# Performance work log

Hardware: AMD Instinct MI355X
Metric: run time of the kernel (lower is better)

The kernel has to match this reference:

```python
import jax, jax.numpy as jnp
import numpy as np

N, E, F_IN, D, H = 20000, 640000, 128, 16, 8  # nodes, edges, in_features, out_features, n_heads


def _linear_params(k, fan_in, fan_out):
    W = jax.random.normal(k, (fan_in, fan_out), jnp.float32) / np.sqrt(fan_in)
    b = jnp.zeros((fan_out,), jnp.float32)
    return W, b


def setup_inputs() -> dict:
    key = jax.random.key(0)
    ks = jax.random.split(key, 8)
    x = jax.random.normal(ks[0], (N, F_IN), jnp.float32)
    edge_index = jax.random.randint(ks[1], (2, E), 0, N, dtype=jnp.int64)
    Wq, bq = _linear_params(ks[2], F_IN, D * H)
    Wk, bk = _linear_params(ks[3], F_IN, D * H)
    Wv, bv = _linear_params(ks[4], F_IN, D * H)
    Wpsi, bpsi = _linear_params(ks[5], D, D)
    Wo, bo = _linear_params(ks[6], D * H * 2, F_IN)
    gamma = jnp.ones((F_IN,), jnp.float32)
    beta = jnp.zeros((F_IN,), jnp.float32)
    return {"x": x, "edge_index": edge_index, "Wq": Wq, "bq": bq, "Wk": Wk, "bk": bk,
            "Wv": Wv, "bv": bv, "Wpsi": Wpsi, "bpsi": bpsi, "Wo": Wo, "bo": bo,
            "gamma": gamma, "beta": beta}


def _segment_softmax(logits, seg, num_segments):
    # numerically-stable softmax of edge logits grouped by destination node (row)
    m = jax.ops.segment_max(logits, seg, num_segments=num_segments)  # [N,H]
    m = jnp.where(jnp.isfinite(m), m, 0.0)
    e = jnp.exp(logits - m[seg])  # [E,H]
    s = jax.ops.segment_sum(e, seg, num_segments=num_segments)  # [N,H]
    return e / (s[seg] + 1e-16)


def reference(x, edge_index, Wq, bq, Wk, bk, Wv, bv, Wpsi, bpsi, Wo, bo, gamma, beta):
    q = (x @ Wq + bq).reshape(N, H, D)
    k = (x @ Wk + bk).reshape(N, H, D)
    v = (x @ Wv + bv).reshape(N, H, D)
    row, col = edge_index[0], edge_index[1]

    logits = jnp.einsum('ehd,ehd->eh', q[row], k[col]) / np.sqrt(D)  # [E,H]
    alpha = _segment_softmax(logits, row, N)  # [E,H]

    v_j = v[col]  # [E,H,D]
    h_lp = jax.ops.segment_sum((alpha[..., None] * v_j).reshape(E, H * D), row, num_segments=N)
    v_bp = jnp.tanh(v_j @ Wpsi + bpsi)  # per-head linear on last dim, [E,H,D]
    h_bp = jax.ops.segment_sum((alpha[..., None] * v_bp).reshape(E, H * D), row, num_segments=N)

    h_out = jnp.concatenate([h_lp, h_bp], axis=1) @ Wo + bo  # [N,F_IN]
    y = x + jax.nn.relu(h_out)
    mu = jnp.mean(y, axis=-1, keepdims=True)
    var = jnp.mean(jnp.square(y - mu), axis=-1, keepdims=True)
    return (y - mu) * jax.lax.rsqrt(var + 1e-5) * gamma + beta
```

## Files before the change

kernel.cpp:

```cpp
#include <hip/hip_runtime.h>
#include <hip/hip_bf16.h>
#include <math.h>

#define NN 20000
#define EE 640000

typedef __attribute__((ext_vector_type(8))) short short8;
typedef __attribute__((ext_vector_type(4))) float f32x4;
typedef __hip_bfloat16 bf16;
typedef __hip_bfloat162 bf162;

__device__ inline ushort f2bf(float f) {
  bf16 h = __float2bfloat16(f);
  return *(ushort*)&h;
}
__device__ inline float2 ldbf2(const ushort* p) {
  return __bfloat1622float2(*(const bf162*)p);
}

__global__ __launch_bounds__(256) void qkv_mfma(
    const float* __restrict__ x,
    const float* __restrict__ Wq, const float* __restrict__ bq,
    const float* __restrict__ Wk, const float* __restrict__ bk,
    const float* __restrict__ Wv, const float* __restrict__ bv,
    float* __restrict__ qbuf, ushort* __restrict__ kvb) {
  __shared__ ushort As[128 * 136];
  __shared__ ushort Bts[128 * 136];
  int t = threadIdx.x;
  int n0 = blockIdx.x * 128;
  int mat = blockIdx.y;
  const float* W    = mat == 0 ? Wq : (mat == 1 ? Wk : Wv);
  const float* bias = mat == 0 ? bq : (mat == 1 ? bk : bv);

  {
    int r = t >> 1, half = (t & 1) * 64;
    int n = n0 + r;
    ushort* dst = &As[r * 136 + half];
    if (n < NN) {
      const float* src = x + (size_t)n * 128 + half;
#pragma unroll
      for (int j = 0; j < 8; ++j) {
        float4 f0 = *(const float4*)(src + 8 * j);
        float4 f1 = *(const float4*)(src + 8 * j + 4);
        ushort tmp[8] = {f2bf(f0.x), f2bf(f0.y), f2bf(f0.z), f2bf(f0.w),
                         f2bf(f1.x), f2bf(f1.y), f2bf(f1.z), f2bf(f1.w)};
        *(uint4*)(dst + 8 * j) = *(uint4*)tmp;
      }
    } else {
#pragma unroll
      for (int j = 0; j < 8; ++j) *(uint4*)(dst + 8 * j) = make_uint4(0, 0, 0, 0);
    }
  }
  {
    int k = t >> 1, nh = (t & 1) * 64;
    const float* src = W + (size_t)k * 128 + nh;
#pragma unroll
    for (int i = 0; i < 16; ++i) {
      float4 f = *(const float4*)(src + 4 * i);
      Bts[(nh + 4 * i + 0) * 136 + k] = f2bf(f.x);
      Bts[(nh + 4 * i + 1) * 136 + k] = f2bf(f.y);
      Bts[(nh + 4 * i + 2) * 136 + k] = f2bf(f.z);
      Bts[(nh + 4 * i + 3) * 136 + k] = f2bf(f.w);
    }
  }
  __syncthreads();

  int w = t >> 6, lane = t & 63;
  int m = lane & 15, q = lane >> 4;
  int r0 = w * 32;
  f32x4 acc0[8], acc1[8];
#pragma unroll
  for (int c = 0; c < 8; ++c) {
    acc0[c] = (f32x4){0.f, 0.f, 0.f, 0.f};
    acc1[c] = (f32x4){0.f, 0.f, 0.f, 0.f};
  }
#pragma unroll
  for (int kb = 0; kb < 4; ++kb) {
    int kof = kb * 32 + 8 * q;
    short8 a0 = *(const short8*)&As[(r0 + m) * 136 + kof];
    short8 a1 = *(const short8*)&As[(r0 + 16 + m) * 136 + kof];
#pragma unroll
    for (int c = 0; c < 8; ++c) {
      short8 b = *(const short8*)&Bts[(c * 16 + m) * 136 + kof];
      acc0[c] = __builtin_amdgcn_mfma_f32_16x16x32_bf16(a0, b, acc0[c], 0, 0, 0);
      acc1[c] = __builtin_amdgcn_mfma_f32_16x16x32_bf16(a1, b, acc1[c], 0, 0, 0);
    }
  }
  int koff = (mat == 2) ? 128 : 0;
#pragma unroll
  for (int c = 0; c < 8; ++c) {
    int col = c * 16 + m;
    float bb = bias[col];
#pragma unroll
    for (int reg = 0; reg < 4; ++reg) {
      int row0 = n0 + r0 + 4 * q + reg;
      int row1 = row0 + 16;
      float v0 = acc0[c][reg] + bb;
      float v1 = acc1[c][reg] + bb;
      if (mat == 0) {
        if (row0 < NN) qbuf[(size_t)row0 * 128 + col] = v0;
        if (row1 < NN) qbuf[(size_t)row1 * 128 + col] = v1;
      } else {
        if (row0 < NN) kvb[(size_t)row0 * 384 + koff + col] = f2bf(v0);
        if (row1 < NN) kvb[(size_t)row1 * 384 + koff + col] = f2bf(v1);
      }
    }
  }
}

__global__ __launch_bounds__(256) void vb_kernel(
    ushort* __restrict__ kvb,
    const float* __restrict__ Wpsi, const float* __restrict__ bpsi) {
  __shared__ float Ws[256];
  __shared__ float bs[16];
  int t = threadIdx.x;
  Ws[t] = Wpsi[t];
  if (t < 16) bs[t] = bpsi[t];
  __syncthreads();
  int idx = blockIdx.x * 256 + t;
  int n = idx >> 3, h = idx & 7;
  ushort* base = kvb + (size_t)n * 384;
  const ushort* vp = base + 128 + h * 16;
  float v[16];
#pragma unroll
  for (int j = 0; j < 8; ++j) {
    float2 f = ldbf2(vp + 2 * j);
    v[2 * j] = f.x; v[2 * j + 1] = f.y;
  }
  float o[16];
#pragma unroll
  for (int d = 0; d < 16; ++d) o[d] = bs[d];
#pragma unroll
  for (int dp = 0; dp < 16; ++dp) {
    float vv = v[dp];
#pragma unroll
    for (int d = 0; d < 16; ++d) o[d] = fmaf(vv, Ws[dp * 16 + d], o[d]);
  }
  ushort* dst = base + 256 + h * 16;
#pragma unroll
  for (int j = 0; j < 8; ++j) {
    uint u = (uint)f2bf(tanhf(o[2 * j])) | ((uint)f2bf(tanhf(o[2 * j + 1])) << 16);
    *(uint*)(dst + 2 * j) = u;
  }
}

__global__ __launch_bounds__(256) void scatter_pad(const int* __restrict__ ei,
                                                   int* __restrict__ cursor,
                                                   int* __restrict__ scol) {
  int e = blockIdx.x * 256 + threadIdx.x;
  if (e < EE) {
    int r = ei[e];
    int c = ei[EE + e];
    int pos = atomicAdd(&cursor[r], 1);
    if (pos < 128) scol[r * 128 + pos] = c;
  }
}

__global__ __launch_bounds__(256) void aggregate_kernel(
    const float* __restrict__ qbuf, const ushort* __restrict__ kvb,
    const int* __restrict__ cursor, const int* __restrict__ scol,
    float* __restrict__ hbuf) {
  int wid = threadIdx.x >> 6, lane = threadIdx.x & 63;
  int node = blockIdx.x * 4 + wid;
  int h = lane >> 3, dg = (lane & 7) * 2;
  int off = h * 16 + dg;
  const float SC = 0.25f * 1.44269504f;
  float2 q2 = *(const float2*)(qbuf + (size_t)node * 128 + off);
  q2.x *= SC; q2.y *= SC;
  int cnt = cursor[node];
  cnt = cnt > 128 ? 128 : cnt;
  int base = node * 128;
  float s = 0.f, aV0 = 0.f, aV1 = 0.f, aB0 = 0.f, aB1 = 0.f;

  auto proc = [&](int j) {
    const ushort* B = kvb + (size_t)j * 384 + off;
    float2 kk = ldbf2(B);
    float2 vv = ldbf2(B + 128);
    float2 tb = ldbf2(B + 256);
    float d = fmaf(q2.x, kk.x, q2.y * kk.y);
    d += __shfl_xor(d, 1);
    d += __shfl_xor(d, 2);
    d += __shfl_xor(d, 4);
    float wgt = exp2f(d);
    s += wgt;
    aV0 = fmaf(wgt, vv.x, aV0); aV1 = fmaf(wgt, vv.y, aV1);
    aB0 = fmaf(wgt, tb.x, aB0); aB1 = fmaf(wgt, tb.y, aB1);
  };
  int i = 0;
  for (; i + 4 <= cnt; i += 4) {
    int4 js = *(const int4*)&scol[base + i];
    proc(js.x); proc(js.y); proc(js.z); proc(js.w);
  }
  for (; i < cnt; ++i) proc(scol[base + i]);

  float inv = s > 0.f ? 1.f / s : 0.f;
  float* hp = hbuf + (size_t)node * 256 + off;
  *(float2*)(hp)       = make_float2(aV0 * inv, aV1 * inv);
  *(float2*)(hp + 128) = make_float2(aB0 * inv, aB1 * inv);
}

__global__ __launch_bounds__(256) void output_mfma(
    const float* __restrict__ hbuf, const float* __restrict__ x,
    const float* __restrict__ Wo, const float* __restrict__ bo,
    const float* __restrict__ gamma, const float* __restrict__ beta,
    float* __restrict__ out) {
  __shared__ ushort As[128 * 136];
  __shared__ ushort Bts[128 * 136];
  __shared__ float bos[128], gs[128], bts[128];
  int t = threadIdx.x;
  int n0 = blockIdx.x * 128;
  if (t < 128) { bos[t] = bo[t]; gs[t] = gamma[t]; bts[t] = beta[t]; }
  int w = t >> 6, lane = t & 63;
  int m = lane & 15, q = lane >> 4;
  int r0 = w * 32;
  f32x4 acc0[8], acc1[8];
#pragma unroll
  for (int c = 0; c < 8; ++c) {
    acc0[c] = (f32x4){0.f, 0.f, 0.f, 0.f};
    acc1[c] = (f32x4){0.f, 0.f, 0.f, 0.f};
  }
  for (int kc = 0; kc < 2; ++kc) {
    if (kc) __syncthreads();
    {
      int r = t >> 1, half = (t & 1) * 64;
      int n = n0 + r;
      ushort* dst = &As[r * 136 + half];
      if (n < NN) {
        const float* src = hbuf + (size_t)n * 256 + kc * 128 + half;
#pragma unroll
        for (int j = 0; j < 8; ++j) {
          float4 f0 = *(const float4*)(src + 8 * j);
          float4 f1 = *(const float4*)(src + 8 * j + 4);
          ushort tmp[8] = {f2bf(f0.x), f2bf(f0.y), f2bf(f0.z), f2bf(f0.w),
                           f2bf(f1.x), f2bf(f1.y), f2bf(f1.z), f2bf(f1.w)};
          *(uint4*)(dst + 8 * j) = *(uint4*)tmp;
        }
      } else {
#pragma unroll
        for (int j = 0; j < 8; ++j) *(uint4*)(dst + 8 * j) = make_uint4(0, 0, 0, 0);
      }
    }
    {
      int k = t >> 1, nh = (t & 1) * 64;
      const float* src = Wo + (size_t)(kc * 128 + k) * 128 + nh;
#pragma unroll
      for (int i = 0; i < 16; ++i) {
        float4 f = *(const float4*)(src + 4 * i);
        Bts[(nh + 4 * i + 0) * 136 + k] = f2bf(f.x);
        Bts[(nh + 4 * i + 1) * 136 + k] = f2bf(f.y);
        Bts[(nh + 4 * i + 2) * 136 + k] = f2bf(f.z);
        Bts[(nh + 4 * i + 3) * 136 + k] = f2bf(f.w);
      }
    }
    __syncthreads();
#pragma unroll
    for (int kb = 0; kb < 4; ++kb) {
      int kof = kb * 32 + 8 * q;
      short8 a0 = *(const short8*)&As[(r0 + m) * 136 + kof];
      short8 a1 = *(const short8*)&As[(r0 + 16 + m) * 136 + kof];
#pragma unroll
      for (int c = 0; c < 8; ++c) {
        short8 b = *(const short8*)&Bts[(c * 16 + m) * 136 + kof];
        acc0[c] = __builtin_amdgcn_mfma_f32_16x16x32_bf16(a0, b, acc0[c], 0, 0, 0);
        acc1[c] = __builtin_amdgcn_mfma_f32_16x16x32_bf16(a1, b, acc1[c], 0, 0, 0);
      }
    }
  }
#pragma unroll
  for (int half = 0; half < 2; ++half) {
#pragma unroll
    for (int reg = 0; reg < 4; ++reg) {
      int row = n0 + r0 + half * 16 + 4 * q + reg;
      bool valid = row < NN;
      float vals[8];
      float sum = 0.f;
#pragma unroll
      for (int c = 0; c < 8; ++c) {
        int col = c * 16 + m;
        float a = (half ? acc1[c][reg] : acc0[c][reg]) + bos[col];
        a = fmaxf(a, 0.f);
        float xv = valid ? x[(size_t)row * 128 + col] : 0.f;
        float v = a + xv;
        vals[c] = v;
        sum += v;
      }
      sum += __shfl_xor(sum, 1); sum += __shfl_xor(sum, 2);
      sum += __shfl_xor(sum, 4); sum += __shfl_xor(sum, 8);
      float mean = sum * (1.f / 128.f);
      float ssq = 0.f;
#pragma unroll
      for (int c = 0; c < 8; ++c) {
        float d = vals[c] - mean;
        ssq = fmaf(d, d, ssq);
      }
      ssq += __shfl_xor(ssq, 1); ssq += __shfl_xor(ssq, 2);
      ssq += __shfl_xor(ssq, 4); ssq += __shfl_xor(ssq, 8);
      float rstd = rsqrtf(ssq * (1.f / 128.f) + 1e-5f);
      if (valid) {
#pragma unroll
        for (int c = 0; c < 8; ++c) {
          int col = c * 16 + m;
          out[(size_t)row * 128 + col] = (vals[c] - mean) * rstd * gs[col] + bts[col];
        }
      }
    }
  }
}

extern "C" void kernel_launch(void* const* d_in, const int* in_sizes, int n_in,
                              void* d_out, int out_size, void* d_ws, size_t ws_size,
                              hipStream_t stream) {
  const float* x     = (const float*)d_in[0];
  const int*   ei    = (const int*)d_in[1];
  const float* Wq    = (const float*)d_in[2];
  const float* bq    = (const float*)d_in[3];
  const float* Wk    = (const float*)d_in[4];
  const float* bk    = (const float*)d_in[5];
  const float* Wv    = (const float*)d_in[6];
  const float* bv    = (const float*)d_in[7];
  const float* Wpsi  = (const float*)d_in[8];
  const float* bpsi  = (const float*)d_in[9];
  const float* Wo    = (const float*)d_in[10];
  const float* bo    = (const float*)d_in[11];
  const float* gamma = (const float*)d_in[12];
  const float* beta  = (const float*)d_in[13];
  float* out = (float*)d_out;

  char* ws = (char*)d_ws;
  float*  qbuf   = (float*) (ws);
  ushort* kvb    = (ushort*)(ws + 10240000);
  float*  hbuf   = (float*) (ws + 25600000);
  int*    cursor = (int*)   (ws + 46080000);
  int*    scol   = (int*)   (ws + 46160000);

  hipMemsetAsync(cursor, 0, 80000, stream);

  qkv_mfma<<<dim3(157, 3), 256, 0, stream>>>(x, Wq, bq, Wk, bk, Wv, bv, qbuf, kvb);
  vb_kernel<<<625, 256, 0, stream>>>(kvb, Wpsi, bpsi);
  scatter_pad<<<2500, 256, 0, stream>>>(ei, cursor, scol);
  aggregate_kernel<<<5000, 256, 0, stream>>>(qbuf, kvb, cursor, scol, hbuf);
  output_mfma<<<157, 256, 0, stream>>>(hbuf, x, Wo, bo, gamma, beta, out);
}
```

Baseline: 229.1 us.

## Pre-convert inputs to bf16, fold Wpsi into V GEMM, restructure aggregation

Adds a prep kernel that converts x and the weight matrices to bf16 in transposed layout once, so the MFMA kernels read fragments straight from global memory without LDS staging. The separate psi kernel is removed by precomputing Wv@Wpsi and a combined bias, which lets a fourth qkv GEMM slice produce tanh(v@Wpsi) directly. Aggregation now gives each lane group one edge with 16-wide vector loads, reduces across lanes with shuffles at the end, and writes h in bf16 to halve that traffic. The costs are an extra launch, an extra pass over x, rounding the folded weights to bf16, and direct global fragment loads in the GEMMs that may be less coalesced.

```diff
diff --git a/kernel.cpp b/kernel.cpp
--- a/kernel.cpp
+++ b/kernel.cpp
@@ -8,66 +8,127 @@
 typedef __attribute__((ext_vector_type(8))) short short8;
 typedef __attribute__((ext_vector_type(4))) float f32x4;
 typedef __hip_bfloat16 bf16;
-typedef __hip_bfloat162 bf162;
 
 __device__ inline ushort f2bf(float f) {
   bf16 h = __float2bfloat16(f);
   return *(ushort*)&h;
 }
-__device__ inline float2 ldbf2(const ushort* p) {
-  return __bfloat1622float2(*(const bf162*)p);
+__device__ inline float bflo(uint u) { return __uint_as_float(u << 16); }
+__device__ inline float bfhi(uint u) { return __uint_as_float(u & 0xFFFF0000u); }
+
+__global__ __launch_bounds__(256) void prep_kernel(
+    const float* __restrict__ x,
+    const float* __restrict__ Wq, const float* __restrict__ Wk,
+    const float* __restrict__ Wv, const float* __restrict__ Wo,
+    const float* __restrict__ Wpsi, const float* __restrict__ bpsi,
+    const float* __restrict__ bv,
+    ushort* __restrict__ xb, ushort* __restrict__ Wts ,
+    ushort* __restrict__ Wot, float* __restrict__ bvpsi) {
+  __shared__ float T[128][129];
+  __shared__ float WpsiS[256];
+  __shared__ float bpsiS[16];
+  int b = blockIdx.x, t = threadIdx.x;
+
+  if (b < 1250) {
+    int idx = b * 2048 + t * 8;
+    const float* src = x + idx;
+    float4 f0 = *(const float4*)(src);
+    float4 f1 = *(const float4*)(src + 4);
+    ushort tmp[8] = {f2bf(f0.x), f2bf(f0.y), f2bf(f0.z), f2bf(f0.w),
+                     f2bf(f1.x), f2bf(f1.y), f2bf(f1.z), f2bf(f1.w)};
+    *(uint4*)(xb + idx) = *(uint4*)tmp;
+    return;
+  }
+
+  if (b <= 1254) {
+    int which = b - 1250;
+    const float* W;
+    int k0 = 0;
+    if (which < 3) W = (which == 0) ? Wq : (which == 1 ? Wk : Wv);
+    else { W = Wo; k0 = (which - 3) * 128; }
+    {
+      int r = t >> 1, c0 = (t & 1) * 64;
+      const float* src = W + (size_t)(k0 + r) * 128 + c0;
+#pragma unroll
+      for (int j = 0; j < 16; ++j) {
+        float4 f = *(const float4*)(src + 4 * j);
+        T[r][c0 + 4 * j + 0] = f.x; T[r][c0 + 4 * j + 1] = f.y;
+        T[r][c0 + 4 * j + 2] = f.z; T[r][c0 + 4 * j + 3] = f.w;
+      }
+    }
+    __syncthreads();
+    int n = t >> 1, kh = (t & 1) * 64;
+    if (which < 3) {
+      ushort* dst = Wts + which * 16384 + n * 128 + kh;
+#pragma unroll
+      for (int j8 = 0; j8 < 8; ++j8) {
+        ushort buf[8];
+#pragma unroll
+        for (int j = 0; j < 8; ++j) buf[j] = f2bf(T[kh + j8 * 8 + j][n]);
+        *(uint4*)(dst + j8 * 8) = *(uint4*)buf;
+      }
+    } else {
+      ushort* dst = Wot + n * 256 + k0 + kh;
+#pragma unroll
+      for (int j8 = 0; j8 < 8; ++j8) {
+        ushort buf[8];
+#pragma unroll
+        for (int j = 0; j < 8; ++j) buf[j] = f2bf(T[kh + j8 * 8 + j][n]);
+        *(uint4*)(dst + j8 * 8) = *(uint4*)buf;
+      }
+    }
+    return;
+  }
+
+  {
+    int r = t >> 1, c0 = (t & 1) * 64;
+    const float* src = Wv + (size_t)r * 128 + c0;
+#pragma unroll
+    for (int j = 0; j < 16; ++j) {
+      float4 f = *(const float4*)(src + 4 * j);
+      T[r][c0 + 4 * j + 0] = f.x; T[r][c0 + 4 * j + 1] = f.y;
+      T[r][c0 + 4 * j + 2] = f.z; T[r][c0 + 4 * j + 3] = f.w;
+    }
+    WpsiS[t] = Wpsi[t];
+    if (t < 16) bpsiS[t] = bpsi[t];
+  }
+  __syncthreads();
+  {
+    int n = t >> 1, kh = (t & 1) * 64;
+    int h = n >> 4, d = n & 15;
+    ushort* dst = Wts + 3 * 16384 + n * 128 + kh;
+    for (int k = 0; k < 64; ++k) {
+      float acc = 0.f;
+#pragma unroll
+      for (int dp = 0; dp < 16; ++dp)
+        acc = fmaf(T[kh + k][h * 16 + dp], WpsiS[dp * 16 + d], acc);
+      dst[k] = f2bf(acc);
+    }
+    if (t < 128) {
+      int hh = t >> 4, dd = t & 15;
+      float acc = bpsiS[dd];
+#pragma unroll
+      for (int dp = 0; dp < 16; ++dp)
+        acc = fmaf(bv[hh * 16 + dp], WpsiS[dp * 16 + dd], acc);
+      bvpsi[t] = acc;
+    }
+  }
 }
 
 __global__ __launch_bounds__(256) void qkv_mfma(
-    const float* __restrict__ x,
-    const float* __restrict__ Wq, const float* __restrict__ bq,
-    const float* __restrict__ Wk, const float* __restrict__ bk,
-    const float* __restrict__ Wv, const float* __restrict__ bv,
+    const ushort* __restrict__ xb, const ushort* __restrict__ Wts,
+    const float* __restrict__ bq, const float* __restrict__ bk,
+    const float* __restrict__ bv, const float* __restrict__ bvpsi,
     float* __restrict__ qbuf, ushort* __restrict__ kvb) {
-  __shared__ ushort As[128 * 136];
-  __shared__ ushort Bts[128 * 136];
   int t = threadIdx.x;
+  int w = t >> 6, lane = t & 63;
+  int m = lane & 15, qd = lane >> 4;
   int n0 = blockIdx.x * 128;
   int mat = blockIdx.y;
-  const float* W    = mat == 0 ? Wq : (mat == 1 ? Wk : Wv);
-  const float* bias = mat == 0 ? bq : (mat == 1 ? bk : bv);
-
-  {
-    int r = t >> 1, half = (t & 1) * 64;
-    int n = n0 + r;
-    ushort* dst = &As[r * 136 + half];
-    if (n < NN) {
-      const float* src = x + (size_t)n * 128 + half;
-#pragma unroll
-      for (int j = 0; j < 8; ++j) {
-        float4 f0 = *(const float4*)(src + 8 * j);
-        float4 f1 = *(const float4*)(src + 8 * j + 4);
-        ushort tmp[8] = {f2bf(f0.x), f2bf(f0.y), f2bf(f0.z), f2bf(f0.w),
-                         f2bf(f1.x), f2bf(f1.y), f2bf(f1.z), f2bf(f1.w)};
-        *(uint4*)(dst + 8 * j) = *(uint4*)tmp;
-      }
-    } else {
-#pragma unroll
-      for (int j = 0; j < 8; ++j) *(uint4*)(dst + 8 * j) = make_uint4(0, 0, 0, 0);
-    }
-  }
-  {
-    int k = t >> 1, nh = (t & 1) * 64;
-    const float* src = W + (size_t)k * 128 + nh;
-#pragma unroll
-    for (int i = 0; i < 16; ++i) {
-      float4 f = *(const float4*)(src + 4 * i);
-      Bts[(nh + 4 * i + 0) * 136 + k] = f2bf(f.x);
-      Bts[(nh + 4 * i + 1) * 136 + k] = f2bf(f.y);
-      Bts[(nh + 4 * i + 2) * 136 + k] = f2bf(f.z);
-      Bts[(nh + 4 * i + 3) * 136 + k] = f2bf(f.w);
-    }
-  }
-  __syncthreads();
-
-  int w = t >> 6, lane = t & 63;
-  int m = lane & 15, q = lane >> 4;
-  int r0 = w * 32;
+  const ushort* Wt = Wts + mat * 16384;
+  const float* bias = (mat == 0) ? bq : (mat == 1 ? bk : (mat == 2 ? bv : bvpsi));
+  int gr0 = n0 + w * 32;
+
   f32x4 acc0[8], acc1[8];
 #pragma unroll
   for (int c = 0; c < 8; ++c) {
@@ -76,71 +137,38 @@
   }
 #pragma unroll
   for (int kb = 0; kb < 4; ++kb) {
-    int kof = kb * 32 + 8 * q;
-    short8 a0 = *(const short8*)&As[(r0 + m) * 136 + kof];
-    short8 a1 = *(const short8*)&As[(r0 + 16 + m) * 136 + kof];
+    int ko = kb * 32 + qd * 8;
+    short8 a0 = *(const short8*)(xb + (size_t)(gr0 + m) * 128 + ko);
+    short8 a1 = *(const short8*)(xb + (size_t)(gr0 + 16 + m) * 128 + ko);
 #pragma unroll
     for (int c = 0; c < 8; ++c) {
-      short8 b = *(const short8*)&Bts[(c * 16 + m) * 136 + kof];
-      acc0[c] = __builtin_amdgcn_mfma_f32_16x16x32_bf16(a0, b, acc0[c], 0, 0, 0);
-      acc1[c] = __builtin_amdgcn_mfma_f32_16x16x32_bf16(a1, b, acc1[c], 0, 0, 0);
-    }
-  }
-  int koff = (mat == 2) ? 128 : 0;
+      short8 bfr = *(const short8*)(Wt + (size_t)(c * 16 + m) * 128 + ko);
+      acc0[c] = __builtin_amdgcn_mfma_f32_16x16x32_bf16(a0, bfr, acc0[c], 0, 0, 0);
+      acc1[c] = __builtin_amdgcn_mfma_f32_16x16x32_bf16(a1, bfr, acc1[c], 0, 0, 0);
+    }
+  }
 #pragma unroll
   for (int c = 0; c < 8; ++c) {
     int col = c * 16 + m;
     float bb = bias[col];
 #pragma unroll
     for (int reg = 0; reg < 4; ++reg) {
-      int row0 = n0 + r0 + 4 * q + reg;
+      int row0 = gr0 + 4 * qd + reg;
       int row1 = row0 + 16;
       float v0 = acc0[c][reg] + bb;
       float v1 = acc1[c][reg] + bb;
       if (mat == 0) {
         if (row0 < NN) qbuf[(size_t)row0 * 128 + col] = v0;
         if (row1 < NN) qbuf[(size_t)row1 * 128 + col] = v1;
+      } else if (mat < 3) {
+        int off = (mat == 1) ? 0 : 128;
+        if (row0 < NN) kvb[(size_t)row0 * 384 + off + col] = f2bf(v0);
+        if (row1 < NN) kvb[(size_t)row1 * 384 + off + col] = f2bf(v1);
       } else {
-        if (row0 < NN) kvb[(size_t)row0 * 384 + koff + col] = f2bf(v0);
-        if (row1 < NN) kvb[(size_t)row1 * 384 + koff + col] = f2bf(v1);
-      }
-    }
-  }
-}
-
-__global__ __launch_bounds__(256) void vb_kernel(
-    ushort* __restrict__ kvb,
-    const float* __restrict__ Wpsi, const float* __restrict__ bpsi) {
-  __shared__ float Ws[256];
-  __shared__ float bs[16];
-  int t = threadIdx.x;
-  Ws[t] = Wpsi[t];
-  if (t < 16) bs[t] = bpsi[t];
-  __syncthreads();
-  int idx = blockIdx.x * 256 + t;
-  int n = idx >> 3, h = idx & 7;
-  ushort* base = kvb + (size_t)n * 384;
-  const ushort* vp = base + 128 + h * 16;
-  float v[16];
-#pragma unroll
-  for (int j = 0; j < 8; ++j) {
-    float2 f = ldbf2(vp + 2 * j);
-    v[2 * j] = f.x; v[2 * j + 1] = f.y;
-  }
-  float o[16];
-#pragma unroll
-  for (int d = 0; d < 16; ++d) o[d] = bs[d];
-#pragma unroll
-  for (int dp = 0; dp < 16; ++dp) {
-    float vv = v[dp];
-#pragma unroll
-    for (int d = 0; d < 16; ++d) o[d] = fmaf(vv, Ws[dp * 16 + d], o[d]);
-  }
-  ushort* dst = base + 256 + h * 16;
-#pragma unroll
-  for (int j = 0; j < 8; ++j) {
-    uint u = (uint)f2bf(tanhf(o[2 * j])) | ((uint)f2bf(tanhf(o[2 * j + 1])) << 16);
-    *(uint*)(dst + 2 * j) = u;
+        if (row0 < NN) kvb[(size_t)row0 * 384 + 256 + col] = f2bf(tanhf(v0));
+        if (row1 < NN) kvb[(size_t)row1 * 384 + 256 + col] = f2bf(tanhf(v1));
+      }
+    }
   }
 }
 
@@ -159,125 +187,121 @@
 __global__ __launch_bounds__(256) void aggregate_kernel(
     const float* __restrict__ qbuf, const ushort* __restrict__ kvb,
     const int* __restrict__ cursor, const int* __restrict__ scol,
-    float* __restrict__ hbuf) {
+    ushort* __restrict__ hb) {
   int wid = threadIdx.x >> 6, lane = threadIdx.x & 63;
   int node = blockIdx.x * 4 + wid;
-  int h = lane >> 3, dg = (lane & 7) * 2;
-  int off = h * 16 + dg;
+  int e = lane >> 3, h = lane & 7;
   const float SC = 0.25f * 1.44269504f;
-  float2 q2 = *(const float2*)(qbuf + (size_t)node * 128 + off);
-  q2.x *= SC; q2.y *= SC;
+
+  float qv[16];
+  {
+    const float* qp = qbuf + (size_t)node * 128 + h * 16;
+#pragma unroll
+    for (int j = 0; j < 4; ++j) {
+      float4 f = *(const float4*)(qp + 4 * j);
+      qv[4 * j + 0] = f.x * SC; qv[4 * j + 1] = f.y * SC;
+      qv[4 * j + 2] = f.z * SC; qv[4 * j + 3] = f.w * SC;
+    }
+  }
   int cnt = cursor[node];
   cnt = cnt > 128 ? 128 : cnt;
   int base = node * 128;
-  float s = 0.f, aV0 = 0.f, aV1 = 0.f, aB0 = 0.f, aB1 = 0.f;
-
-  auto proc = [&](int j) {
-    const ushort* B = kvb + (size_t)j * 384 + off;
-    float2 kk = ldbf2(B);
-    float2 vv = ldbf2(B + 128);
-    float2 tb = ldbf2(B + 256);
-    float d = fmaf(q2.x, kk.x, q2.y * kk.y);
-    d += __shfl_xor(d, 1);
-    d += __shfl_xor(d, 2);
-    d += __shfl_xor(d, 4);
-    float wgt = exp2f(d);
+
+  float s = 0.f;
+  float accV[16], accB[16];
+#pragma unroll
+  for (int j = 0; j < 16; ++j) { accV[j] = 0.f; accB[j] = 0.f; }
+
+  for (int i0 = 0; i0 < cnt; i0 += 8) {
+    int idx = i0 + e;
+    bool valid = idx < cnt;
+    int col = scol[base + (valid ? idx : 0)];
+    const ushort* B = kvb + (size_t)col * 384 + h * 16;
+    uint4 ka = *(const uint4*)(B);
+    uint4 kb4 = *(const uint4*)(B + 8);
+    uint4 va = *(const uint4*)(B + 128);
+    uint4 vb4 = *(const uint4*)(B + 136);
+    uint4 ta = *(const uint4*)(B + 256);
+    uint4 tb4 = *(const uint4*)(B + 264);
+    uint kk[8] = {ka.x, ka.y, ka.z, ka.w, kb4.x, kb4.y, kb4.z, kb4.w};
+    uint vv[8] = {va.x, va.y, va.z, va.w, vb4.x, vb4.y, vb4.z, vb4.w};
+    uint tt[8] = {ta.x, ta.y, ta.z, ta.w, tb4.x, tb4.y, tb4.z, tb4.w};
+    float d = 0.f;
+#pragma unroll
+    for (int i = 0; i < 8; ++i) {
+      d = fmaf(qv[2 * i], bflo(kk[i]), d);
+      d = fmaf(qv[2 * i + 1], bfhi(kk[i]), d);
+    }
+    float wgt = valid ? exp2f(d) : 0.f;
     s += wgt;
-    aV0 = fmaf(wgt, vv.x, aV0); aV1 = fmaf(wgt, vv.y, aV1);
-    aB0 = fmaf(wgt, tb.x, aB0); aB1 = fmaf(wgt, tb.y, aB1);
-  };
-  int i = 0;
-  for (; i + 4 <= cnt; i += 4) {
-    int4 js = *(const int4*)&scol[base + i];
-    proc(js.x); proc(js.y); proc(js.z); proc(js.w);
-  }
-  for (; i < cnt; ++i) proc(scol[base + i]);
-
+#pragma unroll
+    for (int i = 0; i < 8; ++i) {
+      accV[2 * i]     = fmaf(wgt, bflo(vv[i]), accV[2 * i]);
+      accV[2 * i + 1] = fmaf(wgt, bfhi(vv[i]), accV[2 * i + 1]);
+      accB[2 * i]     = fmaf(wgt, bflo(tt[i]), accB[2 * i]);
+      accB[2 * i + 1] = fmaf(wgt, bfhi(tt[i]), accB[2 * i + 1]);
+    }
+  }
+
+#pragma unroll
+  for (int mask = 8; mask <= 32; mask <<= 1) {
+    s += __shfl_xor(s, mask);
+#pragma unroll
+    for (int j = 0; j < 16; ++j) {
+      accV[j] += __shfl_xor(accV[j], mask);
+      accB[j] += __shfl_xor(accB[j], mask);
+    }
+  }
   float inv = s > 0.f ? 1.f / s : 0.f;
-  float* hp = hbuf + (size_t)node * 256 + off;
-  *(float2*)(hp)       = make_float2(aV0 * inv, aV1 * inv);
-  *(float2*)(hp + 128) = make_float2(aB0 * inv, aB1 * inv);
+  int dg = 2 * e;
+  ushort* hp = hb + (size_t)node * 256 + h * 16 + dg;
+  uint uv = (uint)f2bf(accV[dg] * inv) | ((uint)f2bf(accV[dg + 1] * inv) << 16);
+  uint ub = (uint)f2bf(accB[dg] * inv) | ((uint)f2bf(accB[dg + 1] * inv) << 16);
+  *(uint*)(hp) = uv;
+  *(uint*)(hp + 128) = ub;
 }
 
 __global__ __launch_bounds__(256) void output_mfma(
-    const float* __restrict__ hbuf, const float* __restrict__ x,
-    const float* __restrict__ Wo, const float* __restrict__ bo,
+    const ushort* __restrict__ hb, const ushort* __restrict__ Wot,
+    const float* __restrict__ x, const float* __restrict__ bo,
     const float* __restrict__ gamma, const float* __restrict__ beta,
     float* __restrict__ out) {
-  __shared__ ushort As[128 * 136];
-  __shared__ ushort Bts[128 * 136];
-  __shared__ float bos[128], gs[128], bts[128];
   int t = threadIdx.x;
+  int w = t >> 6, lane = t & 63;
+  int m = lane & 15, qd = lane >> 4;
   int n0 = blockIdx.x * 128;
-  if (t < 128) { bos[t] = bo[t]; gs[t] = gamma[t]; bts[t] = beta[t]; }
-  int w = t >> 6, lane = t & 63;
-  int m = lane & 15, q = lane >> 4;
-  int r0 = w * 32;
+  int gr0 = n0 + w * 32;
+
   f32x4 acc0[8], acc1[8];
 #pragma unroll
   for (int c = 0; c < 8; ++c) {
     acc0[c] = (f32x4){0.f, 0.f, 0.f, 0.f};
     acc1[c] = (f32x4){0.f, 0.f, 0.f, 0.f};
   }
-  for (int kc = 0; kc < 2; ++kc) {
-    if (kc) __syncthreads();
-    {
-      int r = t >> 1, half = (t & 1) * 64;
-      int n = n0 + r;
-      ushort* dst = &As[r * 136 + half];
-      if (n < NN) {
-        const float* src = hbuf + (size_t)n * 256 + kc * 128 + half;
-#pragma unroll
-        for (int j = 0; j < 8; ++j) {
-          float4 f0 = *(const float4*)(src + 8 * j);
-          float4 f1 = *(const float4*)(src + 8 * j + 4);
-          ushort tmp[8] = {f2bf(f0.x), f2bf(f0.y), f2bf(f0.z), f2bf(f0.w),
-                           f2bf(f1.x), f2bf(f1.y), f2bf(f1.z), f2bf(f1.w)};
-          *(uint4*)(dst + 8 * j) = *(uint4*)tmp;
-        }
-      } else {
-#pragma unroll
-        for (int j = 0; j < 8; ++j) *(uint4*)(dst + 8 * j) = make_uint4(0, 0, 0, 0);
-      }
-    }
-    {
-      int k = t >> 1, nh = (t & 1) * 64;
-      const float* src = Wo + (size_t)(kc * 128 + k) * 128 + nh;
-#pragma unroll
-      for (int i = 0; i < 16; ++i) {
-        float4 f = *(const float4*)(src + 4 * i);
-        Bts[(nh + 4 * i + 0) * 136 + k] = f2bf(f.x);
-        Bts[(nh + 4 * i + 1) * 136 + k] = f2bf(f.y);
-        Bts[(nh + 4 * i + 2) * 136 + k] = f2bf(f.z);
-        Bts[(nh + 4 * i + 3) * 136 + k] = f2bf(f.w);
-      }
-    }
-    __syncthreads();
-#pragma unroll
-    for (int kb = 0; kb < 4; ++kb) {
-      int kof = kb * 32 + 8 * q;
-      short8 a0 = *(const short8*)&As[(r0 + m) * 136 + kof];
-      short8 a1 = *(const short8*)&As[(r0 + 16 + m) * 136 + kof];
-#pragma unroll
-      for (int c = 0; c < 8; ++c) {
-        short8 b = *(const short8*)&Bts[(c * 16 + m) * 136 + kof];
-        acc0[c] = __builtin_amdgcn_mfma_f32_16x16x32_bf16(a0, b, acc0[c], 0, 0, 0);
-        acc1[c] = __builtin_amdgcn_mfma_f32_16x16x32_bf16(a1, b, acc1[c], 0, 0, 0);
-      }
+#pragma unroll
+  for (int kb = 0; kb < 8; ++kb) {
+    int ko = kb * 32 + qd * 8;
+    short8 a0 = *(const short8*)(hb + (size_t)(gr0 + m) * 256 + ko);
+    short8 a1 = *(const short8*)(hb + (size_t)(gr0 + 16 + m) * 256 + ko);
+#pragma unroll
+    for (int c = 0; c < 8; ++c) {
+      short8 bfr = *(const short8*)(Wot + (size_t)(c * 16 + m) * 256 + ko);
+      acc0[c] = __builtin_amdgcn_mfma_f32_16x16x32_bf16(a0, bfr, acc0[c], 0, 0, 0);
+      acc1[c] = __builtin_amdgcn_mfma_f32_16x16x32_bf16(a1, bfr, acc1[c], 0, 0, 0);
     }
   }
 #pragma unroll
   for (int half = 0; half < 2; ++half) {
 #pragma unroll
     for (int reg = 0; reg < 4; ++reg) {
-      int row = n0 + r0 + half * 16 + 4 * q + reg;
+      int row = gr0 + half * 16 + 4 * qd + reg;
       bool valid = row < NN;
       float vals[8];
       float sum = 0.f;
 #pragma unroll
       for (int c = 0; c < 8; ++c) {
         int col = c * 16 + m;
-        float a = (half ? acc1[c][reg] : acc0[c][reg]) + bos[col];
+        float a = (half ? acc1[c][reg] : acc0[c][reg]) + bo[col];
         a = fmaxf(a, 0.f);
         float xv = valid ? x[(size_t)row * 128 + col] : 0.f;
         float v = a + xv;
@@ -300,7 +324,8 @@
 #pragma unroll
         for (int c = 0; c < 8; ++c) {
           int col = c * 16 + m;
-          out[(size_t)row * 128 + col] = (vals[c] - mean) * rstd * gs[col] + bts[col];
+          out[(size_t)row * 128 + col] =
+              (vals[c] - mean) * rstd * gamma[col] + beta[col];
         }
       }
     }
@@ -327,17 +352,23 @@
   float* out = (float*)d_out;
 
   char* ws = (char*)d_ws;
-  float*  qbuf   = (float*) (ws);
-  ushort* kvb    = (ushort*)(ws + 10240000);
-  float*  hbuf   = (float*) (ws + 25600000);
-  int*    cursor = (int*)   (ws + 46080000);
-  int*    scol   = (int*)   (ws + 46160000);
+  ushort* xb    = (ushort*)(ws);
+  ushort* Wts   = (ushort*)(ws + 5145600);
+  ushort* Wot   = (ushort*)(ws + 5276672);
+  float*  bvpsi = (float*) (ws + 5342208);
+  float*  qbuf  = (float*) (ws + 5342720);
+  ushort* kvb   = (ushort*)(ws + 15582720);
+  ushort* hb    = (ushort*)(ws + 30942720);
+  int*    cursor= (int*)   (ws + 41232128);
+  int*    scol  = (int*)   (ws + 41312256);
 
   hipMemsetAsync(cursor, 0, 80000, stream);
 
-  qkv_mfma<<<dim3(157, 3), 256, 0, stream>>>(x, Wq, bq, Wk, bk, Wv, bv, qbuf, kvb);
-  vb_kernel<<<625, 256, 0, stream>>>(kvb, Wpsi, bpsi);
+  prep_kernel<<<1256, 256, 0, stream>>>(x, Wq, Wk, Wv, Wo, Wpsi, bpsi, bv,
+                                        xb, Wts, Wot, bvpsi);
+  qkv_mfma<<<dim3(157, 4), 256, 0, stream>>>(xb, Wts, bq, bk, bv, bvpsi,
+                                             qbuf, kvb);
   scatter_pad<<<2500, 256, 0, stream>>>(ei, cursor, scol);
-  aggregate_kernel<<<5000, 256, 0, stream>>>(qbuf, kvb, cursor, scol, hbuf);
-  output_mfma<<<157, 256, 0, stream>>>(hbuf, x, Wo, bo, gamma, beta, out);
-}
+  aggregate_kernel<<<5000, 256, 0, stream>>>(qbuf, kvb, cursor, scol, hb);
+  output_mfma<<<157, 256, 0, stream>>>(hb, Wot, x, bo, gamma, beta, out);
+}
```

New measurement: 247.1 us. +7.9%, slower.
